# Kernel tuning notes

Hardware: AMD Instinct MI355X
Metric: run time of the kernel (lower is better)

Reference implementation:

```python
import jax, jax.numpy as jnp
import numpy as np

N = 30000      # nodes
E = 480000     # edges (no self loops; GATConv adds them)
IN = 256       # in_features
OUT = 128      # out_features == per-head channels (concat=False)
H = 4          # heads
NEG_SLOPE = 0.2


def setup_inputs() -> dict:
    key = jax.random.key(0)
    k = jax.random.split(key, 6)
    x = jax.random.normal(k[0], (N, IN), dtype=jnp.float32)
    src = jax.random.randint(k[1], (E,), 0, N, dtype=jnp.int32)
    # guarantee no self loops (GATConv would strip them before re-adding)
    off = jax.random.randint(k[2], (E,), 1, N, dtype=jnp.int32)
    dst = (src + off) % N
    edge_index = jnp.stack([src, dst])  # [2, E]
    W = jax.random.normal(k[3], (IN, H * OUT), dtype=jnp.float32) / np.float32(np.sqrt(IN))
    att_src = jax.random.normal(k[4], (H, OUT), dtype=jnp.float32) / np.float32(np.sqrt(OUT))
    att_dst = jax.random.normal(k[5], (H, OUT), dtype=jnp.float32) / np.float32(np.sqrt(OUT))
    bias = jnp.zeros((OUT,), dtype=jnp.float32)
    return {"x": x, "edge_index": edge_index, "W": W,
            "att_src": att_src, "att_dst": att_dst, "bias": bias}


def reference(x, edge_index, W, att_src, att_dst, bias):
    n = x.shape[0]
    # dense projection -> per-head features [N, H, C]
    h = (x @ W).reshape(n, H, OUT)
    a_s = jnp.einsum('nhc,hc->nh', h, att_src)  # [N, H]
    a_d = jnp.einsum('nhc,hc->nh', h, att_dst)  # [N, H]
    # add self loops (GATConv default add_self_loops=True)
    loop = jnp.arange(n, dtype=edge_index.dtype)
    src = jnp.concatenate([edge_index[0], loop])  # [Et]
    dst = jnp.concatenate([edge_index[1], loop])  # [Et]
    # per-edge attention logits + LeakyReLU
    alpha = jax.nn.leaky_relu(a_s[src] + a_d[dst], NEG_SLOPE)  # [Et, H]
    # segment softmax over incoming edges of each dst node
    amax = jax.ops.segment_max(alpha, dst, num_segments=n)      # [N, H]
    ex = jnp.exp(alpha - amax[dst])
    denom = jax.ops.segment_sum(ex, dst, num_segments=n)        # [N, H]
    w = ex / denom[dst]                                          # [Et, H]
    # gather source features, weight, scatter-add to dst
    msg = h[src] * w[:, :, None]                                 # [Et, H, C]
    out = jax.ops.segment_sum(msg, dst, num_segments=n)          # [N, H, C]
    # concat=False -> mean over heads, then bias, then module's tanh
    out = out.mean(axis=1) + bias                                # [N, C]
    return jnp.tanh(out)
```

## Files before the change

### kernel.cpp

```cpp
#include <hip/hip_runtime.h>
#include <math.h>

#define IN_F   256
#define OUT_F  128
#define HEADS  4
#define HD     (HEADS * OUT_F)
#define K2     1024
#define NEG    0.2f
#define CAP    64

typedef __attribute__((ext_vector_type(8))) short short8;
typedef __attribute__((ext_vector_type(4))) float f32x4;
typedef __attribute__((ext_vector_type(2))) float f32x2;

typedef __attribute__((address_space(1))) const void* gp_t;
typedef __attribute__((address_space(3))) void* lp_t;

static __device__ __forceinline__ ushort f2bf(float f) {
    union { float f; unsigned u; } v; v.f = f;
    unsigned r = (v.u + 0x7FFFu + ((v.u >> 16) & 1u)) >> 16;
    return (ushort)r;
}
static __device__ __forceinline__ float bflo(unsigned u) {
    union { unsigned u; float f; } v; v.u = u << 16; return v.f;
}
static __device__ __forceinline__ float bfhi(unsigned u) {
    union { unsigned u; float f; } v; v.u = u & 0xFFFF0000u; return v.f;
}

#define PKFMA(D, A, B) asm("v_pk_fma_f32 %0, %1, %2, %0" : "+v"(D) : "v"(A), "v"(B))

__global__ __launch_bounds__(256) void prep(const float* __restrict__ W,
                                            const float* __restrict__ att_src,
                                            const float* __restrict__ att_dst,
                                            const int* __restrict__ src,
                                            const int* __restrict__ dst,
                                            ushort* __restrict__ WT2,
                                            float* __restrict__ va_s,
                                            float* __restrict__ va_d,
                                            int* __restrict__ cursor,
                                            int* __restrict__ table,
                                            int n_edges) {
    const int b = blockIdx.x;
    const int tid = threadIdx.x;
    if (b < 512) {
        int idx = b * 256 + tid;
        int cout = idx >> 10, kk = idx & 1023;
        int h = kk >> 8, c = kk & 255;
        WT2[idx] = f2bf(W[(size_t)c * HD + h * OUT_F + cout]);
    } else if (b < 768) {
        const int lane = tid & 63;
        const int p = (b - 512) * 4 + (tid >> 6);
        const int h = p >> 8;
        const int k = p & 255;
        const float* wr = W + (size_t)k * HD + h * OUT_F;
        float w0 = wr[lane], w1 = wr[lane + 64];
        float s0 = att_src[h * OUT_F + lane], s1 = att_src[h * OUT_F + lane + 64];
        float d0 = att_dst[h * OUT_F + lane], d1 = att_dst[h * OUT_F + lane + 64];
        float ss = w0 * s0 + w1 * s1;
        float sd = w0 * d0 + w1 * d1;
#pragma unroll
        for (int off = 32; off > 0; off >>= 1) {
            ss += __shfl_xor(ss, off, 64);
            sd += __shfl_xor(sd, off, 64);
        }
        if (lane == 0) { va_s[p] = ss; va_d[p] = sd; }
    } else {
        int e = (b - 768) * 256 + tid;
        if (e < n_edges) {
            int d = dst[e];
            int r = atomicAdd(&cursor[d], 1);
            if (r < CAP) table[(size_t)d * CAP + r] = src[e];
        }
    }
}

__global__ __launch_bounds__(256) void fused_x(const float* __restrict__ X,
                                               const float* __restrict__ va_s,
                                               const float* __restrict__ va_d,
                                               ushort* __restrict__ Xb,
                                               float* __restrict__ a_s,
                                               float* __restrict__ a_d,
                                               int n_nodes) {
    const int lane = threadIdx.x & 63;
    const int node = blockIdx.x * 4 + (threadIdx.x >> 6);
    if (node >= n_nodes) return;
    float4 v = *(const float4*)(X + (size_t)node * IN_F + lane * 4);
    ushort4 o; o.x = f2bf(v.x); o.y = f2bf(v.y); o.z = f2bf(v.z); o.w = f2bf(v.w);
    *(ushort4*)(Xb + (size_t)node * IN_F + lane * 4) = o;

    float ps[HEADS], pd[HEADS];
#pragma unroll
    for (int hd = 0; hd < HEADS; ++hd) {
        float4 s4 = *(const float4*)(va_s + hd * IN_F + lane * 4);
        float4 d4 = *(const float4*)(va_d + hd * IN_F + lane * 4);
        ps[hd] = v.x * s4.x + v.y * s4.y + v.z * s4.z + v.w * s4.w;
        pd[hd] = v.x * d4.x + v.y * d4.y + v.z * d4.z + v.w * d4.w;
    }
#pragma unroll
    for (int off = 32; off > 0; off >>= 1) {
#pragma unroll
        for (int hd = 0; hd < HEADS; ++hd) {
            ps[hd] += __shfl_xor(ps[hd], off, 64);
            pd[hd] += __shfl_xor(pd[hd], off, 64);
        }
    }
    if (lane == 0) {
        float4 s4 = make_float4(ps[0], ps[1], ps[2], ps[3]);
        float4 d4 = make_float4(pd[0], pd[1], pd[2], pd[3]);
        *(float4*)(a_s + node * 4) = s4;
        *(float4*)(a_d + node * 4) = d4;
    }
}

#define EDGE(E8)                                                            \
    {                                                                       \
        uint2 u = *(const uint2*)(cons + (E8) * 512);                       \
        float4 wA = *(const float4*)(wp + (E8) * 8);                        \
        float4 wB = *(const float4*)(wp + (E8) * 8 + 4);                    \
        f32x2 f01 = {bflo(u.x), bfhi(u.x)};                                 \
        f32x2 f23 = {bflo(u.y), bfhi(u.y)};                                 \
        f32x2 w0p = {wA.x, wA.y}, w1p = {wA.z, wA.w};                       \
        f32x2 w2p = {wB.x, wB.y}, w3p = {wB.z, wB.w};                       \
        PKFMA(a01[0], f01, w0p); PKFMA(a23[0], f23, w0p);                   \
        PKFMA(a01[1], f01, w1p); PKFMA(a23[1], f23, w1p);                   \
        PKFMA(a01[2], f01, w2p); PKFMA(a23[2], f23, w2p);                   \
        PKFMA(a01[3], f01, w3p); PKFMA(a23[3], f23, w3p);                   \
    }

#define ISSUE(EB, DST)                                                      \
    {                                                                       \
        asm volatile("s_waitcnt lgkmcnt(0)" ::: "memory");                  \
        int s0_ = __shfl(sreg, (EB) + 0, 64);                               \
        int s1_ = __shfl(sreg, (EB) + 1, 64);                               \
        int s2_ = __shfl(sreg, (EB) + 2, 64);                               \
        int s3_ = __shfl(sreg, (EB) + 3, 64);                               \
        int s4_ = __shfl(sreg, (EB) + 4, 64);                               \
        int s5_ = __shfl(sreg, (EB) + 5, 64);                               \
        int s6_ = __shfl(sreg, (EB) + 6, 64);                               \
        int s7_ = __shfl(sreg, (EB) + 7, 64);                               \
        int sa_ = (lane & 32) ? s1_ : s0_;                                  \
        int sb_ = (lane & 32) ? s3_ : s2_;                                  \
        int sc_ = (lane & 32) ? s5_ : s4_;                                  \
        int sd_ = (lane & 32) ? s7_ : s6_;                                  \
        __builtin_amdgcn_global_load_lds((gp_t)(xb16 + (size_t)sa_ * 256),  \
                                         (lp_t)((DST) + 0 * 1024), 16, 0, 0);\
        __builtin_amdgcn_global_load_lds((gp_t)(xb16 + (size_t)sb_ * 256),  \
                                         (lp_t)((DST) + 1 * 1024), 16, 0, 0);\
        __builtin_amdgcn_global_load_lds((gp_t)(xb16 + (size_t)sc_ * 256),  \
                                         (lp_t)((DST) + 2 * 1024), 16, 0, 0);\
        __builtin_amdgcn_global_load_lds((gp_t)(xb16 + (size_t)sd_ * 256),  \
                                         (lp_t)((DST) + 3 * 1024), 16, 0, 0);\
    }

__global__ __launch_bounds__(256) void gat_agg(const ushort* __restrict__ Xb,
                                               const float* __restrict__ a_s,
                                               const float* __restrict__ a_d,
                                               const int* __restrict__ cursor,
                                               const int* __restrict__ table,
                                               ushort* __restrict__ Zb,
                                               int n_nodes) {
    __shared__ ushort xst[4][2][8][256];
    __shared__ f32x2 wse2[4][CAP][4];
    const int lane = threadIdx.x & 63;
    const int wid  = threadIdx.x >> 6;
    const int n = blockIdx.x * 4 + wid;
    if (n >= n_nodes) return;
    int deg = cursor[n]; if (deg > CAP) deg = CAP;
    const int* row = table + (size_t)n * CAP;
    const bool act = lane < deg;
    int sreg = act ? row[lane] : n;

    const ushort* xb16 = Xb + (lane & 31) * 8;
    const uint2* xb2 = (const uint2*)Xb;
    uint2 uself = xb2[(size_t)n * 64 + lane];

    const int ntiles = (deg + 7) >> 3;
    if (ntiles > 0) ISSUE(0, (char*)&xst[wid][0][0][0]);

    const float4 ad4 = *(const float4*)(a_d + n * 4);
    const float4 as4 = *(const float4*)(a_s + n * 4);
    const float ad[4] = {ad4.x, ad4.y, ad4.z, ad4.w};
    float aself[4];
    {
        const float asn[4] = {as4.x, as4.y, as4.z, as4.w};
#pragma unroll
        for (int hd = 0; hd < 4; ++hd) {
            float al0 = asn[hd] + ad[hd];
            aself[hd] = al0 > 0.f ? al0 : NEG * al0;
        }
    }
    float al[4];
    {
        float4 av = *(const float4*)(a_s + (size_t)sreg * 4);
        const float as_[4] = {av.x, av.y, av.z, av.w};
#pragma unroll
        for (int hd = 0; hd < 4; ++hd) {
            float a = as_[hd] + ad[hd];
            a = a > 0.f ? a : NEG * a;
            al[hd] = act ? a : -1e30f;
        }
    }
    float m[4];
#pragma unroll
    for (int hd = 0; hd < 4; ++hd) m[hd] = al[hd];
#pragma unroll
    for (int off = 32; off > 0; off >>= 1)
#pragma unroll
        for (int hd = 0; hd < 4; ++hd)
            m[hd] = fmaxf(m[hd], __shfl_xor(m[hd], off, 64));
#pragma unroll
    for (int hd = 0; hd < 4; ++hd) m[hd] = fmaxf(m[hd], aself[hd]);

    float w[4], den[4];
#pragma unroll
    for (int hd = 0; hd < 4; ++hd) {
        w[hd] = act ? __expf(al[hd] - m[hd]) : 0.f;
        den[hd] = w[hd];
    }
#pragma unroll
    for (int off = 32; off > 0; off >>= 1)
#pragma unroll
        for (int hd = 0; hd < 4; ++hd)
            den[hd] += __shfl_xor(den[hd], off, 64);

    float es[4], rdv[4];
#pragma unroll
    for (int hd = 0; hd < 4; ++hd) {
        es[hd] = __expf(aself[hd] - m[hd]);
        rdv[hd] = 1.f / (den[hd] + es[hd]);
    }

    *(float4*)&wse2[wid][lane][0] = make_float4(w[0], w[0], w[1], w[1]);
    *(float4*)&wse2[wid][lane][2] = make_float4(w[2], w[2], w[3], w[3]);

    f32x2 a01[4], a23[4];
    {
        f32x2 s01 = {bflo(uself.x), bfhi(uself.x)};
        f32x2 s23 = {bflo(uself.y), bfhi(uself.y)};
#pragma unroll
        for (int hd = 0; hd < 4; ++hd) {
            f32x2 eh = {es[hd], es[hd]};
            a01[hd] = s01 * eh;
            a23[hd] = s23 * eh;
        }
    }
#pragma unroll 1
    for (int t = 0; t < ntiles; ++t) {
        if (t + 1 < ntiles) {
            ISSUE((t + 1) * 8, (char*)&xst[wid][(t + 1) & 1][0][0]);
            asm volatile("s_waitcnt vmcnt(4)" ::: "memory");
        } else {
            asm volatile("s_waitcnt vmcnt(0)" ::: "memory");
        }
        const char* cons = (const char*)&xst[wid][t & 1][0][0] + lane * 8;
        const float* wp = (const float*)&wse2[wid][t * 8][0];
        EDGE(0); EDGE(1); EDGE(2); EDGE(3);
        EDGE(4); EDGE(5); EDGE(6); EDGE(7);
    }

    ushort* zr = Zb + (size_t)n * K2;
#pragma unroll
    for (int hd = 0; hd < 4; ++hd) {
        f32x2 r2 = {rdv[hd], rdv[hd]};
        f32x2 z01 = a01[hd] * r2;
        f32x2 z23 = a23[hd] * r2;
        ushort4 z;
        z.x = f2bf(z01.x); z.y = f2bf(z01.y);
        z.z = f2bf(z23.x); z.w = f2bf(z23.y);
        *(ushort4*)(zr + hd * 256 + lane * 4) = z;
    }
}

#define GBM 64
#define GBN 128
#define GBK 64

__global__ __launch_bounds__(256) void gemm2(const ushort* __restrict__ Zb,
                                             const ushort* __restrict__ WT2,
                                             const float* __restrict__ bias,
                                             float* __restrict__ out,
                                             int n_nodes) {
    __shared__ ushort As[2][GBM][GBK];
    __shared__ ushort Bs[2][GBN][GBK];
    const int tid = threadIdx.x;
    const int m0 = blockIdx.y * GBM;
    const int wave = tid >> 6, lane = tid & 63;
    const int wm = (wave & 1) * 32, wn = (wave >> 1) * 64;
    const int l15 = lane & 15, quad = lane >> 4;

    const int rr8 = lane >> 3;
    const int cg  = (lane & 7) ^ rr8;
    const ushort* gA0 = Zb + (size_t)(m0 + wave * 16 + rr8) * K2 + cg * 8;
    const ushort* gA1 = gA0 + 8 * K2;
    const ushort* gB0 = WT2 + (size_t)(wave * 32 + rr8) * K2 + cg * 8;
    const ushort* gB1 = gB0 + 8 * K2;
    const ushort* gB2 = gB0 + 16 * K2;
    const ushort* gB3 = gB0 + 24 * K2;

#define STAGE(T, B)                                                          \
    {                                                                        \
        const int ko_ = (T) * GBK;                                           \
        __builtin_amdgcn_global_load_lds((gp_t)(gA0 + ko_),                  \
            (lp_t)&As[B][wave * 16][0], 16, 0, 0);                           \
        __builtin_amdgcn_global_load_lds((gp_t)(gA1 + ko_),                  \
            (lp_t)&As[B][wave * 16 + 8][0], 16, 0, 0);                       \
        __builtin_amdgcn_global_load_lds((gp_t)(gB0 + ko_),                  \
            (lp_t)&Bs[B][wave * 32][0], 16, 0, 0);                           \
        __builtin_amdgcn_global_load_lds((gp_t)(gB1 + ko_),                  \
            (lp_t)&Bs[B][wave * 32 + 8][0], 16, 0, 0);                       \
        __builtin_amdgcn_global_load_lds((gp_t)(gB2 + ko_),                  \
            (lp_t)&Bs[B][wave * 32 + 16][0], 16, 0, 0);                      \
        __builtin_amdgcn_global_load_lds((gp_t)(gB3 + ko_),                  \
            (lp_t)&Bs[B][wave * 32 + 24][0], 16, 0, 0);                      \
    }

    f32x4 acc[2][4];
#pragma unroll
    for (int i = 0; i < 2; ++i)
#pragma unroll
        for (int j = 0; j < 4; ++j) acc[i][j] = (f32x4){0.f, 0.f, 0.f, 0.f};

    const int NT = K2 / GBK;
    STAGE(0, 0);
#pragma unroll 1
    for (int t = 0; t < NT; ++t) {
        const int b = t & 1;
        if (t + 1 < NT) {
            STAGE(t + 1, b ^ 1);
            asm volatile("s_waitcnt vmcnt(6)" ::: "memory");
        } else {
            asm volatile("s_waitcnt vmcnt(0)" ::: "memory");
        }
        asm volatile("s_barrier" ::: "memory");

#pragma unroll
        for (int tt = 0; tt < 2; ++tt) {
            const int sl = ((tt * 4 + quad) ^ (l15 & 7)) * 8;
            short8 af[2], bf_[4];
#pragma unroll
            for (int fm = 0; fm < 2; ++fm)
                af[fm] = *(const short8*)&As[b][wm + fm * 16 + l15][sl];
#pragma unroll
            for (int fn = 0; fn < 4; ++fn)
                bf_[fn] = *(const short8*)&Bs[b][wn + fn * 16 + l15][sl];
#pragma unroll
            for (int fm = 0; fm < 2; ++fm)
#pragma unroll
                for (int fn = 0; fn < 4; ++fn)
                    acc[fm][fn] = __builtin_amdgcn_mfma_f32_16x16x32_bf16(
                        af[fm], bf_[fn], acc[fm][fn], 0, 0, 0);
        }
        asm volatile("s_barrier" ::: "memory");
    }

    float bcol[4];
#pragma unroll
    for (int fn = 0; fn < 4; ++fn) bcol[fn] = bias[wn + fn * 16 + l15];

#pragma unroll
    for (int fm = 0; fm < 2; ++fm) {
        int gmb = m0 + wm + fm * 16 + quad * 4;
#pragma unroll
        for (int reg = 0; reg < 4; ++reg) {
            int gm = gmb + reg;
            if (gm < n_nodes) {
#pragma unroll
                for (int fn = 0; fn < 4; ++fn) {
                    float o = tanhf(0.25f * acc[fm][fn][reg] + bcol[fn]);
                    out[(size_t)gm * OUT_F + wn + fn * 16 + l15] = o;
                }
            }
        }
    }
}

extern "C" void kernel_launch(void* const* d_in, const int* in_sizes, int n_in,
                              void* d_out, int out_size, void* d_ws, size_t ws_size,
                              hipStream_t stream) {
    const float* x       = (const float*)d_in[0];
    const int*   ei      = (const int*)d_in[1];
    const float* W       = (const float*)d_in[2];
    const float* att_src = (const float*)d_in[3];
    const float* att_dst = (const float*)d_in[4];
    const float* bias    = (const float*)d_in[5];
    float* out = (float*)d_out;

    const int n_nodes = in_sizes[0] / IN_F;
    const int n_edges = in_sizes[1] / 2;
    const int* src = ei;
    const int* dst = ei + n_edges;

    char* ws = (char*)d_ws;
    size_t off = 0;
    auto alloc = [&](size_t bytes) -> void* {
        void* p = ws + off;
        off = (off + bytes + 255) & ~(size_t)255;
        return p;
    };
    ushort* Xb     = (ushort*)alloc((size_t)n_nodes * IN_F * sizeof(ushort));
    ushort* Zb     = (ushort*)alloc((size_t)n_nodes * K2 * sizeof(ushort));
    ushort* WT2    = (ushort*)alloc((size_t)OUT_F * K2 * sizeof(ushort));
    float*  va_s   = (float*)alloc((size_t)HEADS * IN_F * sizeof(float));
    float*  va_d   = (float*)alloc((size_t)HEADS * IN_F * sizeof(float));
    float*  a_s    = (float*)alloc((size_t)n_nodes * HEADS * sizeof(float));
    float*  a_d    = (float*)alloc((size_t)n_nodes * HEADS * sizeof(float));
    int*    cursor = (int*)alloc((size_t)n_nodes * sizeof(int));
    int*    table  = (int*)alloc((size_t)n_nodes * CAP * sizeof(int));
    (void)ws_size; (void)n_in; (void)out_size;

    hipMemsetAsync(cursor, 0, (size_t)n_nodes * sizeof(int), stream);

    const int nebk = (n_edges + 255) / 256;
    prep<<<768 + nebk, 256, 0, stream>>>(W, att_src, att_dst, src, dst,
                                         WT2, va_s, va_d, cursor, table, n_edges);
    fused_x<<<(n_nodes + 3) / 4, 256, 0, stream>>>(x, va_s, va_d, Xb, a_s, a_d, n_nodes);
    gat_agg<<<(n_nodes + 3) / 4, 256, 0, stream>>>(Xb, a_s, a_d, cursor, table,
                                                   Zb, n_nodes);

    dim3 ggrid(1, (n_nodes + GBM - 1) / GBM);
    gemm2<<<ggrid, 256, 0, stream>>>(Zb, WT2, bias, out, n_nodes);
}
```

Baseline: 195.3 us.

## Split aggregation per node across two waves, restructure prep kernels, shrink GEMM M-tile

Each destination node's aggregation now uses two waves, each handling half of the 256 input channels, so 2 nodes per block instead of 4. This doubles the wave count and halves per-wave LDS staging and register accumulators. The memset is folded into a prep kernel, and edge bucketing is merged with the X conversion kernel, removing a launch. The GEMM M-tile drops from 64 to 32 rows for more blocks, which means more redundant loads of B tiles.

New measurement: 204.8 us. 1.05x slower.

```diff
diff --git a/kernel.cpp b/kernel.cpp
--- a/kernel.cpp
+++ b/kernel.cpp
@@ -30,17 +30,14 @@
 
 #define PKFMA(D, A, B) asm("v_pk_fma_f32 %0, %1, %2, %0" : "+v"(D) : "v"(A), "v"(B))
 
-__global__ __launch_bounds__(256) void prep(const float* __restrict__ W,
-                                            const float* __restrict__ att_src,
-                                            const float* __restrict__ att_dst,
-                                            const int* __restrict__ src,
-                                            const int* __restrict__ dst,
-                                            ushort* __restrict__ WT2,
-                                            float* __restrict__ va_s,
-                                            float* __restrict__ va_d,
-                                            int* __restrict__ cursor,
-                                            int* __restrict__ table,
-                                            int n_edges) {
+__global__ __launch_bounds__(256) void prep1(const float* __restrict__ W,
+                                             const float* __restrict__ att_src,
+                                             const float* __restrict__ att_dst,
+                                             ushort* __restrict__ WT2,
+                                             float* __restrict__ va_s,
+                                             float* __restrict__ va_d,
+                                             int* __restrict__ cursor,
+                                             int n_nodes) {
     const int b = blockIdx.x;
     const int tid = threadIdx.x;
     if (b < 512) {
@@ -66,24 +63,35 @@
         }
         if (lane == 0) { va_s[p] = ss; va_d[p] = sd; }
     } else {
-        int e = (b - 768) * 256 + tid;
+        int i = (b - 768) * 256 + tid;
+        if (i < n_nodes) cursor[i] = 0;
+    }
+}
+
+__global__ __launch_bounds__(256) void prep2(const float* __restrict__ X,
+                                             const float* __restrict__ va_s,
+                                             const float* __restrict__ va_d,
+                                             const int* __restrict__ src,
+                                             const int* __restrict__ dst,
+                                             ushort* __restrict__ Xb,
+                                             float* __restrict__ a_s,
+                                             float* __restrict__ a_d,
+                                             int* __restrict__ cursor,
+                                             int* __restrict__ table,
+                                             int n_nodes, int n_edges, int nebk) {
+    const int b = blockIdx.x;
+    const int tid = threadIdx.x;
+    if (b < nebk) {
+        int e = b * 256 + tid;
         if (e < n_edges) {
             int d = dst[e];
             int r = atomicAdd(&cursor[d], 1);
             if (r < CAP) table[(size_t)d * CAP + r] = src[e];
         }
-    }
-}
-
-__global__ __launch_bounds__(256) void fused_x(const float* __restrict__ X,
-                                               const float* __restrict__ va_s,
-                                               const float* __restrict__ va_d,
-                                               ushort* __restrict__ Xb,
-                                               float* __restrict__ a_s,
-                                               float* __restrict__ a_d,
-                                               int n_nodes) {
-    const int lane = threadIdx.x & 63;
-    const int node = blockIdx.x * 4 + (threadIdx.x >> 6);
+        return;
+    }
+    const int lane = tid & 63;
+    const int node = (b - nebk) * 4 + (tid >> 6);
     if (node >= n_nodes) return;
     float4 v = *(const float4*)(X + (size_t)node * IN_F + lane * 4);
     ushort4 o; o.x = f2bf(v.x); o.y = f2bf(v.y); o.z = f2bf(v.z); o.w = f2bf(v.w);
@@ -115,42 +123,25 @@
 
 #define EDGE(E8)                                                            \
     {                                                                       \
-        uint2 u = *(const uint2*)(cons + (E8) * 512);                       \
+        uint u = *(const uint*)(cons + (E8) * 256);                         \
         float4 wA = *(const float4*)(wp + (E8) * 8);                        \
         float4 wB = *(const float4*)(wp + (E8) * 8 + 4);                    \
-        f32x2 f01 = {bflo(u.x), bfhi(u.x)};                                 \
-        f32x2 f23 = {bflo(u.y), bfhi(u.y)};                                 \
+        f32x2 f = {bflo(u), bfhi(u)};                                       \
         f32x2 w0p = {wA.x, wA.y}, w1p = {wA.z, wA.w};                       \
         f32x2 w2p = {wB.x, wB.y}, w3p = {wB.z, wB.w};                       \
-        PKFMA(a01[0], f01, w0p); PKFMA(a23[0], f23, w0p);                   \
-        PKFMA(a01[1], f01, w1p); PKFMA(a23[1], f23, w1p);                   \
-        PKFMA(a01[2], f01, w2p); PKFMA(a23[2], f23, w2p);                   \
-        PKFMA(a01[3], f01, w3p); PKFMA(a23[3], f23, w3p);                   \
+        PKFMA(ah[0], f, w0p); PKFMA(ah[1], f, w1p);                         \
+        PKFMA(ah[2], f, w2p); PKFMA(ah[3], f, w3p);                         \
     }
 
 #define ISSUE(EB, DST)                                                      \
     {                                                                       \
         asm volatile("s_waitcnt lgkmcnt(0)" ::: "memory");                  \
-        int s0_ = __shfl(sreg, (EB) + 0, 64);                               \
-        int s1_ = __shfl(sreg, (EB) + 1, 64);                               \
-        int s2_ = __shfl(sreg, (EB) + 2, 64);                               \
-        int s3_ = __shfl(sreg, (EB) + 3, 64);                               \
-        int s4_ = __shfl(sreg, (EB) + 4, 64);                               \
-        int s5_ = __shfl(sreg, (EB) + 5, 64);                               \
-        int s6_ = __shfl(sreg, (EB) + 6, 64);                               \
-        int s7_ = __shfl(sreg, (EB) + 7, 64);                               \
-        int sa_ = (lane & 32) ? s1_ : s0_;                                  \
-        int sb_ = (lane & 32) ? s3_ : s2_;                                  \
-        int sc_ = (lane & 32) ? s5_ : s4_;                                  \
-        int sd_ = (lane & 32) ? s7_ : s6_;                                  \
-        __builtin_amdgcn_global_load_lds((gp_t)(xb16 + (size_t)sa_ * 256),  \
-                                         (lp_t)((DST) + 0 * 1024), 16, 0, 0);\
-        __builtin_amdgcn_global_load_lds((gp_t)(xb16 + (size_t)sb_ * 256),  \
-                                         (lp_t)((DST) + 1 * 1024), 16, 0, 0);\
-        __builtin_amdgcn_global_load_lds((gp_t)(xb16 + (size_t)sc_ * 256),  \
-                                         (lp_t)((DST) + 2 * 1024), 16, 0, 0);\
-        __builtin_amdgcn_global_load_lds((gp_t)(xb16 + (size_t)sd_ * 256),  \
-                                         (lp_t)((DST) + 3 * 1024), 16, 0, 0);\
+        int ea_ = __shfl(sreg, (EB) + (lane >> 4), 64);                     \
+        int eb_ = __shfl(sreg, (EB) + 4 + (lane >> 4), 64);                 \
+        __builtin_amdgcn_global_load_lds((gp_t)(xb16 + (size_t)ea_ * 256),  \
+                                         (lp_t)(DST), 16, 0, 0);            \
+        __builtin_amdgcn_global_load_lds((gp_t)(xb16 + (size_t)eb_ * 256),  \
+                                         (lp_t)((DST) + 1024), 16, 0, 0);   \
     }
 
 __global__ __launch_bounds__(256) void gat_agg(const ushort* __restrict__ Xb,
@@ -160,20 +151,20 @@
                                                const int* __restrict__ table,
                                                ushort* __restrict__ Zb,
                                                int n_nodes) {
-    __shared__ ushort xst[4][2][8][256];
-    __shared__ f32x2 wse2[4][CAP][4];
+    __shared__ ushort xst[4][2][8][128];
+    __shared__ float wse[4][CAP][8];
     const int lane = threadIdx.x & 63;
     const int wid  = threadIdx.x >> 6;
-    const int n = blockIdx.x * 4 + wid;
+    const int n = blockIdx.x * 2 + (wid >> 1);
+    const int half = wid & 1;
     if (n >= n_nodes) return;
     int deg = cursor[n]; if (deg > CAP) deg = CAP;
     const int* row = table + (size_t)n * CAP;
     const bool act = lane < deg;
     int sreg = act ? row[lane] : n;
 
-    const ushort* xb16 = Xb + (lane & 31) * 8;
-    const uint2* xb2 = (const uint2*)Xb;
-    uint2 uself = xb2[(size_t)n * 64 + lane];
+    const ushort* xb16 = Xb + half * 128 + (lane & 15) * 8;
+    uint uself = *(const uint*)(Xb + (size_t)n * IN_F + half * 128 + lane * 2);
 
     const int ntiles = (deg + 7) >> 3;
     if (ntiles > 0) ISSUE(0, (char*)&xst[wid][0][0][0]);
@@ -231,48 +222,43 @@
         rdv[hd] = 1.f / (den[hd] + es[hd]);
     }
 
-    *(float4*)&wse2[wid][lane][0] = make_float4(w[0], w[0], w[1], w[1]);
-    *(float4*)&wse2[wid][lane][2] = make_float4(w[2], w[2], w[3], w[3]);
-
-    f32x2 a01[4], a23[4];
+    *(float4*)&wse[wid][lane][0] = make_float4(w[0], w[0], w[1], w[1]);
+    *(float4*)&wse[wid][lane][4] = make_float4(w[2], w[2], w[3], w[3]);
+
+    f32x2 ah[4];
     {
-        f32x2 s01 = {bflo(uself.x), bfhi(uself.x)};
-        f32x2 s23 = {bflo(uself.y), bfhi(uself.y)};
+        f32x2 s = {bflo(uself), bfhi(uself)};
 #pragma unroll
         for (int hd = 0; hd < 4; ++hd) {
             f32x2 eh = {es[hd], es[hd]};
-            a01[hd] = s01 * eh;
-            a23[hd] = s23 * eh;
+            ah[hd] = s * eh;
         }
     }
 #pragma unroll 1
     for (int t = 0; t < ntiles; ++t) {
         if (t + 1 < ntiles) {
             ISSUE((t + 1) * 8, (char*)&xst[wid][(t + 1) & 1][0][0]);
-            asm volatile("s_waitcnt vmcnt(4)" ::: "memory");
+            asm volatile("s_waitcnt vmcnt(2)" ::: "memory");
         } else {
             asm volatile("s_waitcnt vmcnt(0)" ::: "memory");
         }
-        const char* cons = (const char*)&xst[wid][t & 1][0][0] + lane * 8;
-        const float* wp = (const float*)&wse2[wid][t * 8][0];
+        const char* cons = (const char*)&xst[wid][t & 1][0][0] + lane * 4;
+        const float* wp = &wse[wid][t * 8][0];
         EDGE(0); EDGE(1); EDGE(2); EDGE(3);
         EDGE(4); EDGE(5); EDGE(6); EDGE(7);
     }
 
-    ushort* zr = Zb + (size_t)n * K2;
+    ushort* zr = Zb + (size_t)n * K2 + half * 128 + lane * 2;
 #pragma unroll
     for (int hd = 0; hd < 4; ++hd) {
         f32x2 r2 = {rdv[hd], rdv[hd]};
-        f32x2 z01 = a01[hd] * r2;
-        f32x2 z23 = a23[hd] * r2;
-        ushort4 z;
-        z.x = f2bf(z01.x); z.y = f2bf(z01.y);
-        z.z = f2bf(z23.x); z.w = f2bf(z23.y);
-        *(ushort4*)(zr + hd * 256 + lane * 4) = z;
-    }
-}
-
-#define GBM 64
+        f32x2 z = ah[hd] * r2;
+        ushort2 zz; zz.x = f2bf(z.x); zz.y = f2bf(z.y);
+        *(ushort2*)(zr + hd * 256) = zz;
+    }
+}
+
+#define GBM 32
 #define GBN 128
 #define GBK 64
 
@@ -286,13 +272,12 @@
     const int tid = threadIdx.x;
     const int m0 = blockIdx.y * GBM;
     const int wave = tid >> 6, lane = tid & 63;
-    const int wm = (wave & 1) * 32, wn = (wave >> 1) * 64;
+    const int wm = (wave & 1) * 16, wn = (wave >> 1) * 64;
     const int l15 = lane & 15, quad = lane >> 4;
 
     const int rr8 = lane >> 3;
     const int cg  = (lane & 7) ^ rr8;
-    const ushort* gA0 = Zb + (size_t)(m0 + wave * 16 + rr8) * K2 + cg * 8;
-    const ushort* gA1 = gA0 + 8 * K2;
+    const ushort* gA0 = Zb + (size_t)(m0 + wave * 8 + rr8) * K2 + cg * 8;
     const ushort* gB0 = WT2 + (size_t)(wave * 32 + rr8) * K2 + cg * 8;
     const ushort* gB1 = gB0 + 8 * K2;
     const ushort* gB2 = gB0 + 16 * K2;
@@ -302,9 +287,7 @@
     {                                                                        \
         const int ko_ = (T) * GBK;                                           \
         __builtin_amdgcn_global_load_lds((gp_t)(gA0 + ko_),                  \
-            (lp_t)&As[B][wave * 16][0], 16, 0, 0);                           \
-        __builtin_amdgcn_global_load_lds((gp_t)(gA1 + ko_),                  \
-            (lp_t)&As[B][wave * 16 + 8][0], 16, 0, 0);                       \
+            (lp_t)&As[B][wave * 8][0], 16, 0, 0);                            \
         __builtin_amdgcn_global_load_lds((gp_t)(gB0 + ko_),                  \
             (lp_t)&Bs[B][wave * 32][0], 16, 0, 0);                           \
         __builtin_amdgcn_global_load_lds((gp_t)(gB1 + ko_),                  \
@@ -315,11 +298,9 @@
             (lp_t)&Bs[B][wave * 32 + 24][0], 16, 0, 0);                      \
     }
 
-    f32x4 acc[2][4];
-#pragma unroll
-    for (int i = 0; i < 2; ++i)
-#pragma unroll
-        for (int j = 0; j < 4; ++j) acc[i][j] = (f32x4){0.f, 0.f, 0.f, 0.f};
+    f32x4 acc[4];
+#pragma unroll
+    for (int j = 0; j < 4; ++j) acc[j] = (f32x4){0.f, 0.f, 0.f, 0.f};
 
     const int NT = K2 / GBK;
     STAGE(0, 0);
@@ -328,7 +309,7 @@
         const int b = t & 1;
         if (t + 1 < NT) {
             STAGE(t + 1, b ^ 1);
-            asm volatile("s_waitcnt vmcnt(6)" ::: "memory");
+            asm volatile("s_waitcnt vmcnt(5)" ::: "memory");
         } else {
             asm volatile("s_waitcnt vmcnt(0)" ::: "memory");
         }
@@ -337,19 +318,15 @@
 #pragma unroll
         for (int tt = 0; tt < 2; ++tt) {
             const int sl = ((tt * 4 + quad) ^ (l15 & 7)) * 8;
-            short8 af[2], bf_[4];
-#pragma unroll
-            for (int fm = 0; fm < 2; ++fm)
-                af[fm] = *(const short8*)&As[b][wm + fm * 16 + l15][sl];
+            short8 af = *(const short8*)&As[b][wm + l15][sl];
+            short8 bf_[4];
 #pragma unroll
             for (int fn = 0; fn < 4; ++fn)
                 bf_[fn] = *(const short8*)&Bs[b][wn + fn * 16 + l15][sl];
 #pragma unroll
-            for (int fm = 0; fm < 2; ++fm)
-#pragma unroll
-                for (int fn = 0; fn < 4; ++fn)
-                    acc[fm][fn] = __builtin_amdgcn_mfma_f32_16x16x32_bf16(
-                        af[fm], bf_[fn], acc[fm][fn], 0, 0, 0);
+            for (int fn = 0; fn < 4; ++fn)
+                acc[fn] = __builtin_amdgcn_mfma_f32_16x16x32_bf16(
+                    af, bf_[fn], acc[fn], 0, 0, 0);
         }
         asm volatile("s_barrier" ::: "memory");
     }
@@ -358,18 +335,15 @@
 #pragma unroll
     for (int fn = 0; fn < 4; ++fn) bcol[fn] = bias[wn + fn * 16 + l15];
 
-#pragma unroll
-    for (int fm = 0; fm < 2; ++fm) {
-        int gmb = m0 + wm + fm * 16 + quad * 4;
-#pragma unroll
-        for (int reg = 0; reg < 4; ++reg) {
-            int gm = gmb + reg;
-            if (gm < n_nodes) {
-#pragma unroll
-                for (int fn = 0; fn < 4; ++fn) {
-                    float o = tanhf(0.25f * acc[fm][fn][reg] + bcol[fn]);
-                    out[(size_t)gm * OUT_F + wn + fn * 16 + l15] = o;
-                }
+    int gmb = m0 + wm + quad * 4;
+#pragma unroll
+    for (int reg = 0; reg < 4; ++reg) {
+        int gm = gmb + reg;
+        if (gm < n_nodes) {
+#pragma unroll
+            for (int fn = 0; fn < 4; ++fn) {
+                float o = tanhf(0.25f * acc[fn][reg] + bcol[fn]);
+                out[(size_t)gm * OUT_F + wn + fn * 16 + l15] = o;
             }
         }
     }
@@ -409,13 +383,15 @@
     int*    table  = (int*)alloc((size_t)n_nodes * CAP * sizeof(int));
     (void)ws_size; (void)n_in; (void)out_size;
 
-    hipMemsetAsync(cursor, 0, (size_t)n_nodes * sizeof(int), stream);
-
+    const int czb  = (n_nodes + 255) / 256;
     const int nebk = (n_edges + 255) / 256;
-    prep<<<768 + nebk, 256, 0, stream>>>(W, att_src, att_dst, src, dst,
-                                         WT2, va_s, va_d, cursor, table, n_edges);
-    fused_x<<<(n_nodes + 3) / 4, 256, 0, stream>>>(x, va_s, va_d, Xb, a_s, a_d, n_nodes);
-    gat_agg<<<(n_nodes + 3) / 4, 256, 0, stream>>>(Xb, a_s, a_d, cursor, table,
+
+    prep1<<<768 + czb, 256, 0, stream>>>(W, att_src, att_dst, WT2, va_s, va_d,
+                                         cursor, n_nodes);
+    prep2<<<nebk + (n_nodes + 3) / 4, 256, 0, stream>>>(x, va_s, va_d, src, dst,
+                                                        Xb, a_s, a_d, cursor, table,
+                                                        n_nodes, n_edges, nebk);
+    gat_agg<<<(n_nodes + 1) / 2, 256, 0, stream>>>(Xb, a_s, a_d, cursor, table,
                                                    Zb, n_nodes);
 
     dim3 ggrid(1, (n_nodes + GBM - 1) / GBM);
```

## Fuse all stages into one cooperative persistent kernel with grid syncs

Applied to the files above, without the earlier changes.

Replaces the memset plus four separate kernel launches with a single cooperative persistent kernel that loops over the work of each stage and separates stages with grid-wide syncs. The cursor zeroing moves into a prep stage, and the edge bucketing moves later next to the bf16 conversion of X. The GEMM tile shrinks from 64 to 32 rows per block, and the aggregation and GEMM shared buffers share one union. The aim is to remove launch gaps and the memset, at the cost of grid.sync overhead and a grid capped at 1024 blocks, which may lower parallelism in the heavy stages. A fallback path with separate kernels is kept.

Result: slower. 393.5 us (+101.5%).

```diff
diff --git a/kernel.cpp b/kernel.cpp
--- a/kernel.cpp
+++ b/kernel.cpp
@@ -1,5 +1,8 @@
 #include <hip/hip_runtime.h>
+#include <hip/hip_cooperative_groups.h>
 #include <math.h>
+
+namespace cgrp = cooperative_groups;
 
 #define IN_F   256
 #define OUT_F  128
@@ -8,6 +11,9 @@
 #define K2     1024
 #define NEG    0.2f
 #define CAP    64
+#define GBM    32
+#define GBN    128
+#define GBK    64
 
 typedef __attribute__((ext_vector_type(8))) short short8;
 typedef __attribute__((ext_vector_type(4))) float f32x4;
@@ -30,19 +36,12 @@
 
 #define PKFMA(D, A, B) asm("v_pk_fma_f32 %0, %1, %2, %0" : "+v"(D) : "v"(A), "v"(B))
 
-__global__ __launch_bounds__(256) void prep(const float* __restrict__ W,
-                                            const float* __restrict__ att_src,
-                                            const float* __restrict__ att_dst,
-                                            const int* __restrict__ src,
-                                            const int* __restrict__ dst,
-                                            ushort* __restrict__ WT2,
-                                            float* __restrict__ va_s,
-                                            float* __restrict__ va_d,
-                                            int* __restrict__ cursor,
-                                            int* __restrict__ table,
-                                            int n_edges) {
-    const int b = blockIdx.x;
-    const int tid = threadIdx.x;
+
+static __device__ __forceinline__ void prep1_body(int b, int tid,
+        const float* __restrict__ W, const float* __restrict__ att_src,
+        const float* __restrict__ att_dst, ushort* __restrict__ WT2,
+        float* __restrict__ va_s, float* __restrict__ va_d,
+        int* __restrict__ cursor, int n_nodes) {
     if (b < 512) {
         int idx = b * 256 + tid;
         int cout = idx >> 10, kk = idx & 1023;
@@ -66,24 +65,29 @@
         }
         if (lane == 0) { va_s[p] = ss; va_d[p] = sd; }
     } else {
-        int e = (b - 768) * 256 + tid;
+        int i = (b - 768) * 256 + tid;
+        if (i < n_nodes) cursor[i] = 0;
+    }
+}
+
+static __device__ __forceinline__ void prep2_body(int b, int tid,
+        const float* __restrict__ X, const float* __restrict__ va_s,
+        const float* __restrict__ va_d, const int* __restrict__ src,
+        const int* __restrict__ dst, ushort* __restrict__ Xb,
+        float* __restrict__ a_s, float* __restrict__ a_d,
+        int* __restrict__ cursor, int* __restrict__ table,
+        int n_nodes, int n_edges, int nebk) {
+    if (b < nebk) {
+        int e = b * 256 + tid;
         if (e < n_edges) {
             int d = dst[e];
             int r = atomicAdd(&cursor[d], 1);
             if (r < CAP) table[(size_t)d * CAP + r] = src[e];
         }
-    }
-}
-
-__global__ __launch_bounds__(256) void fused_x(const float* __restrict__ X,
-                                               const float* __restrict__ va_s,
-                                               const float* __restrict__ va_d,
-                                               ushort* __restrict__ Xb,
-                                               float* __restrict__ a_s,
-                                               float* __restrict__ a_d,
-                                               int n_nodes) {
-    const int lane = threadIdx.x & 63;
-    const int node = blockIdx.x * 4 + (threadIdx.x >> 6);
+        return;
+    }
+    const int lane = tid & 63;
+    const int node = (b - nebk) * 4 + (tid >> 6);
     if (node >= n_nodes) return;
     float4 v = *(const float4*)(X + (size_t)node * IN_F + lane * 4);
     ushort4 o; o.x = f2bf(v.x); o.y = f2bf(v.y); o.z = f2bf(v.z); o.w = f2bf(v.w);
@@ -153,18 +157,12 @@
                                          (lp_t)((DST) + 3 * 1024), 16, 0, 0);\
     }
 
-__global__ __launch_bounds__(256) void gat_agg(const ushort* __restrict__ Xb,
-                                               const float* __restrict__ a_s,
-                                               const float* __restrict__ a_d,
-                                               const int* __restrict__ cursor,
-                                               const int* __restrict__ table,
-                                               ushort* __restrict__ Zb,
-                                               int n_nodes) {
-    __shared__ ushort xst[4][2][8][256];
-    __shared__ f32x2 wse2[4][CAP][4];
-    const int lane = threadIdx.x & 63;
-    const int wid  = threadIdx.x >> 6;
-    const int n = blockIdx.x * 4 + wid;
+static __device__ __forceinline__ void agg_body(int vb, int lane, int wid,
+        ushort (*xst)[2][8][256], float (*wse)[CAP][8],
+        const ushort* __restrict__ Xb, const float* __restrict__ a_s,
+        const float* __restrict__ a_d, const int* __restrict__ cursor,
+        const int* __restrict__ table, ushort* __restrict__ Zb, int n_nodes) {
+    const int n = vb * 4 + wid;
     if (n >= n_nodes) return;
     int deg = cursor[n]; if (deg > CAP) deg = CAP;
     const int* row = table + (size_t)n * CAP;
@@ -175,8 +173,11 @@
     const uint2* xb2 = (const uint2*)Xb;
     uint2 uself = xb2[(size_t)n * 64 + lane];
 
+    char* xb0 = (char*)&xst[wid][0][0][0];
+    char* xb1 = (char*)&xst[wid][1][0][0];
+
     const int ntiles = (deg + 7) >> 3;
-    if (ntiles > 0) ISSUE(0, (char*)&xst[wid][0][0][0]);
+    if (ntiles > 0) ISSUE(0, xb0);
 
     const float4 ad4 = *(const float4*)(a_d + n * 4);
     const float4 as4 = *(const float4*)(a_s + n * 4);
@@ -231,8 +232,8 @@
         rdv[hd] = 1.f / (den[hd] + es[hd]);
     }
 
-    *(float4*)&wse2[wid][lane][0] = make_float4(w[0], w[0], w[1], w[1]);
-    *(float4*)&wse2[wid][lane][2] = make_float4(w[2], w[2], w[3], w[3]);
+    *(float4*)&wse[wid][lane][0] = make_float4(w[0], w[0], w[1], w[1]);
+    *(float4*)&wse[wid][lane][4] = make_float4(w[2], w[2], w[3], w[3]);
 
     f32x2 a01[4], a23[4];
     {
@@ -248,13 +249,13 @@
 #pragma unroll 1
     for (int t = 0; t < ntiles; ++t) {
         if (t + 1 < ntiles) {
-            ISSUE((t + 1) * 8, (char*)&xst[wid][(t + 1) & 1][0][0]);
+            ISSUE((t + 1) * 8, ((t + 1) & 1) ? xb1 : xb0);
             asm volatile("s_waitcnt vmcnt(4)" ::: "memory");
         } else {
             asm volatile("s_waitcnt vmcnt(0)" ::: "memory");
         }
-        const char* cons = (const char*)&xst[wid][t & 1][0][0] + lane * 8;
-        const float* wp = (const float*)&wse2[wid][t * 8][0];
+        const char* cons = ((t & 1) ? xb1 : xb0) + lane * 8;
+        const float* wp = &wse[wid][t * 8][0];
         EDGE(0); EDGE(1); EDGE(2); EDGE(3);
         EDGE(4); EDGE(5); EDGE(6); EDGE(7);
     }
@@ -272,39 +273,11 @@
     }
 }
 
-#define GBM 64
-#define GBN 128
-#define GBK 64
-
-__global__ __launch_bounds__(256) void gemm2(const ushort* __restrict__ Zb,
-                                             const ushort* __restrict__ WT2,
-                                             const float* __restrict__ bias,
-                                             float* __restrict__ out,
-                                             int n_nodes) {
-    __shared__ ushort As[2][GBM][GBK];
-    __shared__ ushort Bs[2][GBN][GBK];
-    const int tid = threadIdx.x;
-    const int m0 = blockIdx.y * GBM;
-    const int wave = tid >> 6, lane = tid & 63;
-    const int wm = (wave & 1) * 32, wn = (wave >> 1) * 64;
-    const int l15 = lane & 15, quad = lane >> 4;
-
-    const int rr8 = lane >> 3;
-    const int cg  = (lane & 7) ^ rr8;
-    const ushort* gA0 = Zb + (size_t)(m0 + wave * 16 + rr8) * K2 + cg * 8;
-    const ushort* gA1 = gA0 + 8 * K2;
-    const ushort* gB0 = WT2 + (size_t)(wave * 32 + rr8) * K2 + cg * 8;
-    const ushort* gB1 = gB0 + 8 * K2;
-    const ushort* gB2 = gB0 + 16 * K2;
-    const ushort* gB3 = gB0 + 24 * K2;
-
 #define STAGE(T, B)                                                          \
     {                                                                        \
         const int ko_ = (T) * GBK;                                           \
         __builtin_amdgcn_global_load_lds((gp_t)(gA0 + ko_),                  \
-            (lp_t)&As[B][wave * 16][0], 16, 0, 0);                           \
-        __builtin_amdgcn_global_load_lds((gp_t)(gA1 + ko_),                  \
-            (lp_t)&As[B][wave * 16 + 8][0], 16, 0, 0);                       \
+            (lp_t)&As[B][wave * 8][0], 16, 0, 0);                            \
         __builtin_amdgcn_global_load_lds((gp_t)(gB0 + ko_),                  \
             (lp_t)&Bs[B][wave * 32][0], 16, 0, 0);                           \
         __builtin_amdgcn_global_load_lds((gp_t)(gB1 + ko_),                  \
@@ -315,11 +288,25 @@
             (lp_t)&Bs[B][wave * 32 + 24][0], 16, 0, 0);                      \
     }
 
-    f32x4 acc[2][4];
-#pragma unroll
-    for (int i = 0; i < 2; ++i)
-#pragma unroll
-        for (int j = 0; j < 4; ++j) acc[i][j] = (f32x4){0.f, 0.f, 0.f, 0.f};
+static __device__ __forceinline__ void gemm_body(int tile, int lane, int wave,
+        ushort (*As)[GBM][GBK], ushort (*Bs)[GBN][GBK],
+        const ushort* __restrict__ Zb, const ushort* __restrict__ WT2,
+        const float* __restrict__ bias, float* __restrict__ out, int n_nodes) {
+    const int m0 = tile * GBM;
+    const int wm = (wave & 1) * 16, wn = (wave >> 1) * 64;
+    const int l15 = lane & 15, quad = lane >> 4;
+
+    const int rr8 = lane >> 3;
+    const int cgx = (lane & 7) ^ rr8;
+    const ushort* gA0 = Zb + (size_t)(m0 + wave * 8 + rr8) * K2 + cgx * 8;
+    const ushort* gB0 = WT2 + (size_t)(wave * 32 + rr8) * K2 + cgx * 8;
+    const ushort* gB1 = gB0 + 8 * K2;
+    const ushort* gB2 = gB0 + 16 * K2;
+    const ushort* gB3 = gB0 + 24 * K2;
+
+    f32x4 acc[4];
+#pragma unroll
+    for (int j = 0; j < 4; ++j) acc[j] = (f32x4){0.f, 0.f, 0.f, 0.f};
 
     const int NT = K2 / GBK;
     STAGE(0, 0);
@@ -328,7 +315,7 @@
         const int b = t & 1;
         if (t + 1 < NT) {
             STAGE(t + 1, b ^ 1);
-            asm volatile("s_waitcnt vmcnt(6)" ::: "memory");
+            asm volatile("s_waitcnt vmcnt(5)" ::: "memory");
         } else {
             asm volatile("s_waitcnt vmcnt(0)" ::: "memory");
         }
@@ -337,19 +324,15 @@
 #pragma unroll
         for (int tt = 0; tt < 2; ++tt) {
             const int sl = ((tt * 4 + quad) ^ (l15 & 7)) * 8;
-            short8 af[2], bf_[4];
-#pragma unroll
-            for (int fm = 0; fm < 2; ++fm)
-                af[fm] = *(const short8*)&As[b][wm + fm * 16 + l15][sl];
+            short8 af = *(const short8*)&As[b][wm + l15][sl];
+            short8 bf_[4];
 #pragma unroll
             for (int fn = 0; fn < 4; ++fn)
                 bf_[fn] = *(const short8*)&Bs[b][wn + fn * 16 + l15][sl];
 #pragma unroll
-            for (int fm = 0; fm < 2; ++fm)
-#pragma unroll
-                for (int fn = 0; fn < 4; ++fn)
-                    acc[fm][fn] = __builtin_amdgcn_mfma_f32_16x16x32_bf16(
-                        af[fm], bf_[fn], acc[fm][fn], 0, 0, 0);
+            for (int fn = 0; fn < 4; ++fn)
+                acc[fn] = __builtin_amdgcn_mfma_f32_16x16x32_bf16(
+                    af, bf_[fn], acc[fn], 0, 0, 0);
         }
         asm volatile("s_barrier" ::: "memory");
     }
@@ -358,21 +341,88 @@
 #pragma unroll
     for (int fn = 0; fn < 4; ++fn) bcol[fn] = bias[wn + fn * 16 + l15];
 
-#pragma unroll
-    for (int fm = 0; fm < 2; ++fm) {
-        int gmb = m0 + wm + fm * 16 + quad * 4;
-#pragma unroll
-        for (int reg = 0; reg < 4; ++reg) {
-            int gm = gmb + reg;
-            if (gm < n_nodes) {
-#pragma unroll
-                for (int fn = 0; fn < 4; ++fn) {
-                    float o = tanhf(0.25f * acc[fm][fn][reg] + bcol[fn]);
-                    out[(size_t)gm * OUT_F + wn + fn * 16 + l15] = o;
-                }
+    int gmb = m0 + wm + quad * 4;
+#pragma unroll
+    for (int reg = 0; reg < 4; ++reg) {
+        int gm = gmb + reg;
+        if (gm < n_nodes) {
+#pragma unroll
+            for (int fn = 0; fn < 4; ++fn) {
+                float o = tanhf(0.25f * acc[fn][reg] + bcol[fn]);
+                out[(size_t)gm * OUT_F + wn + fn * 16 + l15] = o;
             }
         }
     }
+}
+
+struct SharedU {
+    union {
+        struct { ushort xst[4][2][8][256]; float wse[4][CAP][8]; } a;
+        struct { ushort As[2][GBM][GBK]; ushort Bs[2][GBN][GBK]; } g;
+    };
+};
+
+__global__ __launch_bounds__(256, 4) void mega(
+        const float* X, const int* src, const int* dst, const float* W,
+        const float* att_src, const float* att_dst, const float* bias,
+        float* out, ushort* Xb, ushort* Zb, ushort* WT2,
+        float* va_s, float* va_d, float* a_s, float* a_d,
+        int* cursor, int* table, int n_nodes, int n_edges, int nebk, int czb) {
+    __shared__ SharedU sh;
+    cgrp::grid_group grid = cgrp::this_grid();
+    const int tid = threadIdx.x;
+    const int lane = tid & 63, wid = tid >> 6;
+    const int nb = gridDim.x;
+
+    const int NB1 = 768 + czb;
+    for (int b = blockIdx.x; b < NB1; b += nb)
+        prep1_body(b, tid, W, att_src, att_dst, WT2, va_s, va_d, cursor, n_nodes);
+    grid.sync();
+
+    const int NB2 = nebk + (n_nodes + 3) / 4;
+    for (int b = blockIdx.x; b < NB2; b += nb)
+        prep2_body(b, tid, X, va_s, va_d, src, dst, Xb, a_s, a_d,
+                   cursor, table, n_nodes, n_edges, nebk);
+    grid.sync();
+
+    const int NB3 = (n_nodes + 3) / 4;
+    for (int b = blockIdx.x; b < NB3; b += nb)
+        agg_body(b, lane, wid, sh.a.xst, sh.a.wse, Xb, a_s, a_d,
+                 cursor, table, Zb, n_nodes);
+    grid.sync();
+
+    const int NB4 = (n_nodes + GBM - 1) / GBM;
+    for (int t = blockIdx.x; t < NB4; t += nb)
+        gemm_body(t, lane, wid, sh.g.As, sh.g.Bs, Zb, WT2, bias, out, n_nodes);
+}
+
+__global__ __launch_bounds__(256) void k_prep1(const float* W, const float* att_src,
+        const float* att_dst, ushort* WT2, float* va_s, float* va_d,
+        int* cursor, int n_nodes) {
+    prep1_body(blockIdx.x, threadIdx.x, W, att_src, att_dst, WT2, va_s, va_d,
+               cursor, n_nodes);
+}
+__global__ __launch_bounds__(256) void k_prep2(const float* X, const float* va_s,
+        const float* va_d, const int* src, const int* dst, ushort* Xb,
+        float* a_s, float* a_d, int* cursor, int* table,
+        int n_nodes, int n_edges, int nebk) {
+    prep2_body(blockIdx.x, threadIdx.x, X, va_s, va_d, src, dst, Xb, a_s, a_d,
+               cursor, table, n_nodes, n_edges, nebk);
+}
+__global__ __launch_bounds__(256) void k_agg(const ushort* Xb, const float* a_s,
+        const float* a_d, const int* cursor, const int* table, ushort* Zb,
+        int n_nodes) {
+    __shared__ ushort xst[4][2][8][256];
+    __shared__ float wse[4][CAP][8];
+    agg_body(blockIdx.x, threadIdx.x & 63, threadIdx.x >> 6, xst, wse,
+             Xb, a_s, a_d, cursor, table, Zb, n_nodes);
+}
+__global__ __launch_bounds__(256) void k_gemm(const ushort* Zb, const ushort* WT2,
+        const float* bias, float* out, int n_nodes) {
+    __shared__ ushort As[2][GBM][GBK];
+    __shared__ ushort Bs[2][GBN][GBK];
+    gemm_body(blockIdx.y, threadIdx.x & 63, threadIdx.x >> 6, As, Bs,
+              Zb, WT2, bias, out, n_nodes);
 }
 
 extern "C" void kernel_launch(void* const* d_in, const int* in_sizes, int n_in,
@@ -386,8 +436,8 @@
     const float* bias    = (const float*)d_in[5];
     float* out = (float*)d_out;
 
-    const int n_nodes = in_sizes[0] / IN_F;
-    const int n_edges = in_sizes[1] / 2;
+    int n_nodes = in_sizes[0] / IN_F;
+    int n_edges = in_sizes[1] / 2;
     const int* src = ei;
     const int* dst = ei + n_edges;
 
@@ -409,15 +459,37 @@
     int*    table  = (int*)alloc((size_t)n_nodes * CAP * sizeof(int));
     (void)ws_size; (void)n_in; (void)out_size;
 
-    hipMemsetAsync(cursor, 0, (size_t)n_nodes * sizeof(int), stream);
-
-    const int nebk = (n_edges + 255) / 256;
-    prep<<<768 + nebk, 256, 0, stream>>>(W, att_src, att_dst, src, dst,
-                                         WT2, va_s, va_d, cursor, table, n_edges);
-    fused_x<<<(n_nodes + 3) / 4, 256, 0, stream>>>(x, va_s, va_d, Xb, a_s, a_d, n_nodes);
-    gat_agg<<<(n_nodes + 3) / 4, 256, 0, stream>>>(Xb, a_s, a_d, cursor, table,
-                                                   Zb, n_nodes);
-
-    dim3 ggrid(1, (n_nodes + GBM - 1) / GBM);
-    gemm2<<<ggrid, 256, 0, stream>>>(Zb, WT2, bias, out, n_nodes);
-}
+    int czb  = (n_nodes + 255) / 256;
+    int nebk = (n_edges + 255) / 256;
+
+    int maxb = 0;
+    hipError_t oe = hipOccupancyMaxActiveBlocksPerMultiprocessor(
+        &maxb, reinterpret_cast<const void*>(&mega), 256, 0);
+    bool coop_ok = false;
+    if (oe == hipSuccess && maxb >= 1) {
+        int gridb = 256 * maxb;
+        if (gridb > 1024) gridb = 1024;
+        void* args[] = {
+            (void*)&x, (void*)&src, (void*)&dst, (void*)&W,
+            (void*)&att_src, (void*)&att_dst, (void*)&bias, (void*)&out,
+            (void*)&Xb, (void*)&Zb, (void*)&WT2, (void*)&va_s, (void*)&va_d,
+            (void*)&a_s, (void*)&a_d, (void*)&cursor, (void*)&table,
+            (void*)&n_nodes, (void*)&n_edges, (void*)&nebk, (void*)&czb};
+        hipError_t le = hipLaunchCooperativeKernel(
+            reinterpret_cast<const void*>(&mega), dim3(gridb), dim3(256),
+            args, 0, stream);
+        coop_ok = (le == hipSuccess);
+    }
+
+    if (!coop_ok) {
+        k_prep1<<<768 + czb, 256, 0, stream>>>(W, att_src, att_dst, WT2,
+                                               va_s, va_d, cursor, n_nodes);
+        k_prep2<<<nebk + (n_nodes + 3) / 4, 256, 0, stream>>>(
+            x, va_s, va_d, src, dst, Xb, a_s, a_d, cursor, table,
+            n_nodes, n_edges, nebk);
+        k_agg<<<(n_nodes + 3) / 4, 256, 0, stream>>>(Xb, a_s, a_d, cursor,
+                                                     table, Zb, n_nodes);
+        dim3 ggrid(1, (n_nodes + GBM - 1) / GBM);
+        k_gemm<<<ggrid, 256, 0, stream>>>(Zb, WT2, bias, out, n_nodes);
+    }
+}
```
